# Kernel tuning notes

Measured on AMD Instinct MI355X. Metric: run time of the kernel, lower is better.

The kernel has to match this reference:

```python
import jax, jax.numpy as jnp
import numpy as np

EMBED_DIM = 256
IDX = 3
SLOT_NORM = True
NEG = -9e15


def setup_inputs() -> dict:
    key = jax.random.key(0)
    ks = jax.random.split(key, 7)
    B, S, D, N = 16, 8192, EMBED_DIM, 64
    return {
        "input_embedding": jax.random.normal(ks[0], (B, S, D), dtype=jnp.float32),
        "mask": jax.random.randint(ks[1], (B, N, S), 0, 2, dtype=jnp.int32),
        "Wv": jax.random.normal(ks[2], (D, D), dtype=jnp.float32) * 0.02,
        "bv": jax.random.normal(ks[3], (D,), dtype=jnp.float32) * 0.02,
        "Wk": jax.random.normal(ks[4], (D, D), dtype=jnp.float32) * 0.02,
        "bk": jax.random.normal(ks[5], (D,), dtype=jnp.float32) * 0.02,
        "queries": jax.random.normal(ks[6], (N, D), dtype=jnp.float32) * 0.02,
    }


def reference(input_embedding, mask, Wv, bv, Wk, bk, queries):
    # values/keys: [B, S, D] (torch Linear: x @ W.T + b)
    values = jnp.einsum("bsd,ed->bse", input_embedding, Wv) + bv
    keys = jnp.einsum("bsd,ed->bse", input_embedding, Wk) + bk
    # attn_logits: [B, N, S]
    logits = jnp.einsum("nd,bsd->bns", queries, keys) / jnp.sqrt(
        jnp.asarray(EMBED_DIM, dtype=keys.dtype)
    )
    logits = jnp.where(mask == 0, jnp.asarray(NEG, dtype=logits.dtype), logits)
    if SLOT_NORM:
        attn = jax.nn.softmax(logits, axis=-2)  # normalize over slots
        attn = attn / jnp.sum(attn, axis=-1, keepdims=True)
    else:
        attn = jax.nn.softmax(logits, axis=-1)
    attention = attn[:, IDX, :][:, None, :]  # [B, 1, S]
    out = jnp.matmul(attention, values)  # [B, 1, D]
    return out, attention
```

## Files before the change

kernel.cpp:

```cpp
#include <hip/hip_runtime.h>


#define B_ 16
#define S_ 8192
#define D_ 256
#define N_ 64
#define NEG_ (-9e15f)
#define LSTR 264

typedef __attribute__((ext_vector_type(8))) short s8_t;
typedef __attribute__((ext_vector_type(4))) float f4_t;
typedef unsigned int u32;
typedef unsigned short u16;

__device__ __forceinline__ u16 f2bf(float f) {
  u32 u = __builtin_bit_cast(u32, f);
  u += 0x7fffu + ((u >> 16) & 1u);
  return (u16)(u >> 16);
}
__device__ __forceinline__ float bflo(u32 p) { return __builtin_bit_cast(float, p << 16); }
__device__ __forceinline__ float bfhi(u32 p) { return __builtin_bit_cast(float, p & 0xffff0000u); }

__global__ void prep_qk(const float* __restrict__ queries, const float* __restrict__ Wk,
                        const float* __restrict__ bk, u16* __restrict__ qp,
                        float* __restrict__ qb) {
  const int n = blockIdx.x, d = threadIdx.x;
  const float* q = &queries[n * D_];
  float acc = 0.f;
  for (int e = 0; e < D_; ++e) acc = fmaf(q[e], Wk[e * D_ + d], acc);
  qp[n * D_ + d] = f2bf(acc);
  if (d == 0) {
    float s = 0.f;
    for (int e = 0; e < D_; ++e) s = fmaf(q[e], bk[e], s);
    qb[n] = s;
  }
}

__global__ __launch_bounds__(256, 2) void attn_main(
    const float* __restrict__ x, const int* __restrict__ mask,
    const u16* __restrict__ qp, const float* __restrict__ qb,
    float* __restrict__ wsum, float* __restrict__ denom, float* __restrict__ att) {
  __shared__ u16 q_lds[N_ * LSTR];
  __shared__ u16 in_lds[64 * LSTR];
  __shared__ u32 pm[4 * 64];

  const int t = threadIdx.x;
  const int lane = t & 63;
  const int w = t >> 6;
  const int c15 = lane & 15;
  const int g = lane >> 4;
  const int b = blockIdx.y;
  const int sbase = blockIdx.x * 256;

  {
    const int n = t >> 2, q = t & 3;
#pragma unroll
    for (int j = 0; j < 8; ++j)
      *(uint4*)&q_lds[n * LSTR + q * 64 + j * 8] = *(const uint4*)&qp[n * D_ + q * 64 + j * 8];
  }
  float qbv[4];
#pragma unroll
  for (int t4 = 0; t4 < 4; ++t4) qbv[t4] = qb[t4 * 16 + c15];

  f4_t wacc = {0.f, 0.f, 0.f, 0.f};
  float dacc = 0.f;

  for (int tt = 0; tt < 4; ++tt) {
    const int s0 = sbase + tt * 64;
    __syncthreads();
    {
      const int col = (t & 63) * 4;
#pragma unroll
      for (int it = 0; it < 16; ++it) {
        const int row = it * 4 + w;
        const float4 v = *(const float4*)&x[(((long)b * S_) + s0 + row) * D_ + col];
        uint2 h;
        h.x = (u32)f2bf(v.x) | ((u32)f2bf(v.y) << 16);
        h.y = (u32)f2bf(v.z) | ((u32)f2bf(v.w) << 16);
        *(uint2*)&in_lds[row * LSTR + col] = h;
      }
      const int s = t & 63, p = t >> 6;
      const int* mrow = mask + ((long)b * N_ + p * 16) * S_ + s0 + s;
      u32 bits = 0;
#pragma unroll
      for (int i = 0; i < 16; ++i) bits |= (u32)(mrow[i * S_] != 0) << i;
      pm[p * 64 + s] = bits;
    }
    __syncthreads();

    f4_t acc[4] = {{0.f,0.f,0.f,0.f},{0.f,0.f,0.f,0.f},{0.f,0.f,0.f,0.f},{0.f,0.f,0.f,0.f}};
    const u16* arow = &in_lds[(16 * w + c15) * LSTR + g * 8];
    const u16* br0 = &q_lds[(0 + c15) * LSTR + g * 8];
    const u16* br1 = &q_lds[(16 + c15) * LSTR + g * 8];
    const u16* br2 = &q_lds[(32 + c15) * LSTR + g * 8];
    const u16* br3 = &q_lds[(48 + c15) * LSTR + g * 8];
#pragma unroll
    for (int c = 0; c < 8; ++c) {
      const s8_t a = *(const s8_t*)&arow[c * 32];
      acc[0] = __builtin_amdgcn_mfma_f32_16x16x32_bf16(a, *(const s8_t*)&br0[c * 32], acc[0], 0, 0, 0);
      acc[1] = __builtin_amdgcn_mfma_f32_16x16x32_bf16(a, *(const s8_t*)&br1[c * 32], acc[1], 0, 0, 0);
      acc[2] = __builtin_amdgcn_mfma_f32_16x16x32_bf16(a, *(const s8_t*)&br2[c * 32], acc[2], 0, 0, 0);
      acc[3] = __builtin_amdgcn_mfma_f32_16x16x32_bf16(a, *(const s8_t*)&br3[c * 32], acc[3], 0, 0, 0);
    }

    float unorm[4];
#pragma unroll
    for (int r = 0; r < 4; ++r) {
      const int sl = 16 * w + g * 4 + r;
      float lf[4];
#pragma unroll
      for (int t4 = 0; t4 < 4; ++t4)
        lf[t4] = ((pm[t4 * 64 + sl] >> c15) & 1) ? (acc[t4][r] + qbv[t4]) * 0.0625f : NEG_;
      float m = fmaxf(fmaxf(lf[0], lf[1]), fmaxf(lf[2], lf[3]));
      m = fmaxf(m, __shfl_xor(m, 1));
      m = fmaxf(m, __shfl_xor(m, 2));
      m = fmaxf(m, __shfl_xor(m, 4));
      m = fmaxf(m, __shfl_xor(m, 8));
      const float e0 = __expf(lf[0] - m);
      float sm = e0 + __expf(lf[1] - m) + __expf(lf[2] - m) + __expf(lf[3] - m);
      sm += __shfl_xor(sm, 1);
      sm += __shfl_xor(sm, 2);
      sm += __shfl_xor(sm, 4);
      sm += __shfl_xor(sm, 8);
      const float e3 = __shfl(e0, (lane & 48) | 3);
      unorm[r] = e3 / sm;
    }
    if (c15 == 3) {
      f4_t u = {unorm[0], unorm[1], unorm[2], unorm[3]};
      *(f4_t*)&att[(long)b * S_ + s0 + 16 * w + g * 4] = u;
    }
#pragma unroll
    for (int r = 0; r < 4; ++r) {
#pragma unroll
      for (int gg = 0; gg < 4; ++gg) {
        const float a_s = __shfl(unorm[r], gg * 16);
        const uint2 h = *(const uint2*)&in_lds[(16 * w + gg * 4 + r) * LSTR + lane * 4];
        wacc[0] = fmaf(a_s, bflo(h.x), wacc[0]);
        wacc[1] = fmaf(a_s, bfhi(h.x), wacc[1]);
        wacc[2] = fmaf(a_s, bflo(h.y), wacc[2]);
        wacc[3] = fmaf(a_s, bfhi(h.y), wacc[3]);
        dacc += a_s;
      }
    }
  }
#pragma unroll
  for (int j = 0; j < 4; ++j) atomicAdd(&wsum[b * D_ + lane * 4 + j], wacc[j]);
  if (lane == 0) atomicAdd(&denom[b], dacc);
}

__global__ void finalize_k(const float* __restrict__ wsum, const float* __restrict__ denom,
                           const float* __restrict__ Wv, const float* __restrict__ bv,
                           float* __restrict__ out, float* __restrict__ att) {
  __shared__ float wl[D_];
  const int b = blockIdx.x, t = threadIdx.x;
  wl[t] = wsum[b * D_ + t];
  __syncthreads();
  const float dn = denom[b];
  float o = 0.f;
  const float* wr = &Wv[t * D_];
  for (int e = 0; e < D_; ++e) o = fmaf(wl[e], wr[e], o);
  out[b * D_ + t] = o / dn + bv[t];
  const float inv = 1.0f / dn;
  for (int s = t; s < S_; s += 256) att[(long)b * S_ + s] *= inv;
}

extern "C" void kernel_launch(void* const* d_in, const int* in_sizes, int n_in,
                              void* d_out, int out_size, void* d_ws, size_t ws_size,
                              hipStream_t stream) {
  const float* x = (const float*)d_in[0];
  const int* mask = (const int*)d_in[1];
  const float* Wv = (const float*)d_in[2];
  const float* bv = (const float*)d_in[3];
  const float* Wk = (const float*)d_in[4];
  const float* bk = (const float*)d_in[5];
  const float* queries = (const float*)d_in[6];

  char* ws = (char*)d_ws;
  u16* qp = (u16*)ws;
  float* qb = (float*)(ws + 32768);
  float* wsum = (float*)(ws + 33024);
  float* denom = (float*)(ws + 49408);
  float* out = (float*)d_out;
  float* att = out + B_ * D_;

  hipMemsetAsync(wsum, 0, 16384 + 64, stream);
  prep_qk<<<N_, D_, 0, stream>>>(queries, Wk, bk, qp, qb);
  attn_main<<<dim3(32, B_), 256, 0, stream>>>(x, mask, qp, qb, wsum, denom, att);
  finalize_k<<<B_, D_, 0, stream>>>(wsum, denom, Wv, bv, out, att);
}
```

Baseline: 270.3 us.

## Double grid, drop query LDS staging, replace atomics with per-block partials

The main kernel now handles 128 positions per block instead of 256 and launches 64x16 blocks. The query matrix is pre-swizzled into MFMA fragment order so each lane reads its operands straight from global memory, which removes the query LDS buffer and raises occupancy to 4 blocks per CU. Global atomics and the memset are replaced by per-block partial sums that are reduced in LDS and written out, and finalize gains a second grid dimension so it can rescale attention in parallel. The prep kernel is restructured to use LDS and a tree reduction. In exchange, query fragments are re-read from global or cache by every block, and finalize must reduce 64 partials per batch.

```diff
diff --git a/kernel.cpp b/kernel.cpp
--- a/kernel.cpp
+++ b/kernel.cpp
@@ -22,27 +22,37 @@
 __device__ __forceinline__ float bfhi(u32 p) { return __builtin_bit_cast(float, p & 0xffff0000u); }
 
 __global__ void prep_qk(const float* __restrict__ queries, const float* __restrict__ Wk,
-                        const float* __restrict__ bk, u16* __restrict__ qp,
+                        const float* __restrict__ bk, u16* __restrict__ qf,
                         float* __restrict__ qb) {
+  __shared__ float ql[D_];
+  __shared__ float rb[D_];
   const int n = blockIdx.x, d = threadIdx.x;
-  const float* q = &queries[n * D_];
-  float acc = 0.f;
-  for (int e = 0; e < D_; ++e) acc = fmaf(q[e], Wk[e * D_ + d], acc);
-  qp[n * D_ + d] = f2bf(acc);
-  if (d == 0) {
-    float s = 0.f;
-    for (int e = 0; e < D_; ++e) s = fmaf(q[e], bk[e], s);
-    qb[n] = s;
+  const float qv = queries[n * D_ + d];
+  ql[d] = qv;
+  rb[d] = qv * bk[d];
+  __syncthreads();
+  float a0 = 0.f, a1 = 0.f, a2 = 0.f, a3 = 0.f;
+#pragma unroll 4
+  for (int e = 0; e < D_; e += 4) {
+    a0 = fmaf(ql[e + 0], Wk[(e + 0) * D_ + d], a0);
+    a1 = fmaf(ql[e + 1], Wk[(e + 1) * D_ + d], a1);
+    a2 = fmaf(ql[e + 2], Wk[(e + 2) * D_ + d], a2);
+    a3 = fmaf(ql[e + 3], Wk[(e + 3) * D_ + d], a3);
   }
-}
-
-__global__ __launch_bounds__(256, 2) void attn_main(
+  const float acc = (a0 + a1) + (a2 + a3);
+  const int t4 = n >> 4, c15 = n & 15, c = d >> 5, g = (d >> 3) & 3, j = d & 7;
+  qf[((t4 * 8 + c) * 64 + g * 16 + c15) * 8 + j] = f2bf(acc);
+  for (int s = 128; s > 0; s >>= 1) { __syncthreads(); if (d < s) rb[d] += rb[d + s]; }
+  if (d == 0) qb[n] = rb[0];
+}
+
+__global__ __launch_bounds__(256, 4) void attn_main(
     const float* __restrict__ x, const int* __restrict__ mask,
-    const u16* __restrict__ qp, const float* __restrict__ qb,
-    float* __restrict__ wsum, float* __restrict__ denom, float* __restrict__ att) {
-  __shared__ u16 q_lds[N_ * LSTR];
-  __shared__ u16 in_lds[64 * LSTR];
+    const u16* __restrict__ qf, const float* __restrict__ qb,
+    float* __restrict__ pw, float* __restrict__ dpart, float* __restrict__ att) {
+  __shared__ __align__(16) u16 in_lds[64 * LSTR];
   __shared__ u32 pm[4 * 64];
+  float* ldsW = (float*)in_lds;
 
   const int t = threadIdx.x;
   const int lane = t & 63;
@@ -50,22 +60,16 @@
   const int c15 = lane & 15;
   const int g = lane >> 4;
   const int b = blockIdx.y;
-  const int sbase = blockIdx.x * 256;
-
-  {
-    const int n = t >> 2, q = t & 3;
-#pragma unroll
-    for (int j = 0; j < 8; ++j)
-      *(uint4*)&q_lds[n * LSTR + q * 64 + j * 8] = *(const uint4*)&qp[n * D_ + q * 64 + j * 8];
-  }
-  float qbv[4];
-#pragma unroll
-  for (int t4 = 0; t4 < 4; ++t4) qbv[t4] = qb[t4 * 16 + c15];
+  const int sb = blockIdx.x;
+  const int sbase = sb * 128;
+
+  const float qbv0 = qb[c15], qbv1 = qb[16 + c15], qbv2 = qb[32 + c15], qbv3 = qb[48 + c15];
+  const s8_t* qfs = (const s8_t*)qf;
 
   f4_t wacc = {0.f, 0.f, 0.f, 0.f};
   float dacc = 0.f;
 
-  for (int tt = 0; tt < 4; ++tt) {
+  for (int tt = 0; tt < 2; ++tt) {
     const int s0 = sbase + tt * 64;
     __syncthreads();
     {
@@ -80,7 +84,7 @@
         *(uint2*)&in_lds[row * LSTR + col] = h;
       }
       const int s = t & 63, p = t >> 6;
-      const int* mrow = mask + ((long)b * N_ + p * 16) * S_ + s0 + s;
+      const int* mrow = mask + ((long)b * N_ + p * 16) * S_ + sbase + tt * 64 + s;
       u32 bits = 0;
 #pragma unroll
       for (int i = 0; i < 16; ++i) bits |= (u32)(mrow[i * S_] != 0) << i;
@@ -88,36 +92,39 @@
     }
     __syncthreads();
 
-    f4_t acc[4] = {{0.f,0.f,0.f,0.f},{0.f,0.f,0.f,0.f},{0.f,0.f,0.f,0.f},{0.f,0.f,0.f,0.f}};
     const u16* arow = &in_lds[(16 * w + c15) * LSTR + g * 8];
-    const u16* br0 = &q_lds[(0 + c15) * LSTR + g * 8];
-    const u16* br1 = &q_lds[(16 + c15) * LSTR + g * 8];
-    const u16* br2 = &q_lds[(32 + c15) * LSTR + g * 8];
-    const u16* br3 = &q_lds[(48 + c15) * LSTR + g * 8];
+    f4_t acc0 = {0.f,0.f,0.f,0.f}, acc1 = {0.f,0.f,0.f,0.f};
+    f4_t acc2 = {0.f,0.f,0.f,0.f}, acc3 = {0.f,0.f,0.f,0.f};
 #pragma unroll
     for (int c = 0; c < 8; ++c) {
-      const s8_t a = *(const s8_t*)&arow[c * 32];
-      acc[0] = __builtin_amdgcn_mfma_f32_16x16x32_bf16(a, *(const s8_t*)&br0[c * 32], acc[0], 0, 0, 0);
-      acc[1] = __builtin_amdgcn_mfma_f32_16x16x32_bf16(a, *(const s8_t*)&br1[c * 32], acc[1], 0, 0, 0);
-      acc[2] = __builtin_amdgcn_mfma_f32_16x16x32_bf16(a, *(const s8_t*)&br2[c * 32], acc[2], 0, 0, 0);
-      acc[3] = __builtin_amdgcn_mfma_f32_16x16x32_bf16(a, *(const s8_t*)&br3[c * 32], acc[3], 0, 0, 0);
+      const s8_t a  = *(const s8_t*)&arow[c * 32];
+      const s8_t b0 = qfs[(0 * 8 + c) * 64 + lane];
+      const s8_t b1 = qfs[(1 * 8 + c) * 64 + lane];
+      const s8_t b2 = qfs[(2 * 8 + c) * 64 + lane];
+      const s8_t b3 = qfs[(3 * 8 + c) * 64 + lane];
+      acc0 = __builtin_amdgcn_mfma_f32_16x16x32_bf16(a, b0, acc0, 0, 0, 0);
+      acc1 = __builtin_amdgcn_mfma_f32_16x16x32_bf16(a, b1, acc1, 0, 0, 0);
+      acc2 = __builtin_amdgcn_mfma_f32_16x16x32_bf16(a, b2, acc2, 0, 0, 0);
+      acc3 = __builtin_amdgcn_mfma_f32_16x16x32_bf16(a, b3, acc3, 0, 0, 0);
     }
 
     float unorm[4];
 #pragma unroll
     for (int r = 0; r < 4; ++r) {
       const int sl = 16 * w + g * 4 + r;
-      float lf[4];
-#pragma unroll
-      for (int t4 = 0; t4 < 4; ++t4)
-        lf[t4] = ((pm[t4 * 64 + sl] >> c15) & 1) ? (acc[t4][r] + qbv[t4]) * 0.0625f : NEG_;
-      float m = fmaxf(fmaxf(lf[0], lf[1]), fmaxf(lf[2], lf[3]));
+      const u32 m0 = pm[0 * 64 + sl], m1 = pm[1 * 64 + sl];
+      const u32 m2 = pm[2 * 64 + sl], m3 = pm[3 * 64 + sl];
+      const float lf0 = ((m0 >> c15) & 1) ? (acc0[r] + qbv0) * 0.0625f : NEG_;
+      const float lf1 = ((m1 >> c15) & 1) ? (acc1[r] + qbv1) * 0.0625f : NEG_;
+      const float lf2 = ((m2 >> c15) & 1) ? (acc2[r] + qbv2) * 0.0625f : NEG_;
+      const float lf3 = ((m3 >> c15) & 1) ? (acc3[r] + qbv3) * 0.0625f : NEG_;
+      float m = fmaxf(fmaxf(lf0, lf1), fmaxf(lf2, lf3));
       m = fmaxf(m, __shfl_xor(m, 1));
       m = fmaxf(m, __shfl_xor(m, 2));
       m = fmaxf(m, __shfl_xor(m, 4));
       m = fmaxf(m, __shfl_xor(m, 8));
-      const float e0 = __expf(lf[0] - m);
-      float sm = e0 + __expf(lf[1] - m) + __expf(lf[2] - m) + __expf(lf[3] - m);
+      const float e0 = __expf(lf0 - m);
+      float sm = e0 + __expf(lf1 - m) + __expf(lf2 - m) + __expf(lf3 - m);
       sm += __shfl_xor(sm, 1);
       sm += __shfl_xor(sm, 2);
       sm += __shfl_xor(sm, 4);
@@ -129,6 +136,7 @@
       f4_t u = {unorm[0], unorm[1], unorm[2], unorm[3]};
       *(f4_t*)&att[(long)b * S_ + s0 + 16 * w + g * 4] = u;
     }
+
 #pragma unroll
     for (int r = 0; r < 4; ++r) {
 #pragma unroll
@@ -143,25 +151,65 @@
       }
     }
   }
-#pragma unroll
-  for (int j = 0; j < 4; ++j) atomicAdd(&wsum[b * D_ + lane * 4 + j], wacc[j]);
-  if (lane == 0) atomicAdd(&denom[b], dacc);
-}
-
-__global__ void finalize_k(const float* __restrict__ wsum, const float* __restrict__ denom,
+
+  __syncthreads();
+  if (t < 64) { f4_t z = {0.f,0.f,0.f,0.f}; *(f4_t*)&ldsW[t * 4] = z; }
+  if (t == 64) ldsW[D_] = 0.f;
+  __syncthreads();
+#pragma unroll
+  for (int j = 0; j < 4; ++j) atomicAdd(&ldsW[lane * 4 + j], wacc[j]);
+  if (lane == 0) atomicAdd(&ldsW[D_], dacc);
+  __syncthreads();
+  const int blk = b * 64 + sb;
+  if (t < D_) pw[(long)blk * D_ + t] = ldsW[t];
+  if (t == 0) dpart[blk] = ldsW[D_];
+}
+
+__global__ void finalize_k(const float* __restrict__ pw, const float* __restrict__ dpart,
                            const float* __restrict__ Wv, const float* __restrict__ bv,
                            float* __restrict__ out, float* __restrict__ att) {
+  __shared__ float red[64];
   __shared__ float wl[D_];
-  const int b = blockIdx.x, t = threadIdx.x;
-  wl[t] = wsum[b * D_ + t];
-  __syncthreads();
-  const float dn = denom[b];
-  float o = 0.f;
-  const float* wr = &Wv[t * D_];
-  for (int e = 0; e < D_; ++e) o = fmaf(wl[e], wr[e], o);
-  out[b * D_ + t] = o / dn + bv[t];
-  const float inv = 1.0f / dn;
-  for (int s = t; s < S_; s += 256) att[(long)b * S_ + s] *= inv;
+  const int b = blockIdx.x, t = threadIdx.x, part = blockIdx.y;
+  if (t < 64) red[t] = dpart[b * 64 + t];
+  __syncthreads();
+  if (t < 32) red[t] += red[t + 32];
+  __syncthreads();
+  if (t < 16) red[t] += red[t + 16];
+  __syncthreads();
+  if (t < 8) red[t] += red[t + 8];
+  __syncthreads();
+  if (t < 4) red[t] += red[t + 4];
+  __syncthreads();
+  if (t < 2) red[t] += red[t + 2];
+  __syncthreads();
+  if (t == 0) red[0] += red[1];
+  __syncthreads();
+  const float dn = red[0];
+  if (part == 0) {
+    float s0 = 0.f, s1 = 0.f, s2 = 0.f, s3 = 0.f;
+    const float* p = pw + (long)b * 64 * D_ + t;
+#pragma unroll 4
+    for (int sb = 0; sb < 64; sb += 4) {
+      s0 += p[(sb + 0) * D_]; s1 += p[(sb + 1) * D_];
+      s2 += p[(sb + 2) * D_]; s3 += p[(sb + 3) * D_];
+    }
+    wl[t] = (s0 + s1) + (s2 + s3);
+    __syncthreads();
+    const float4* wr = (const float4*)&Wv[t * D_];
+    const float4* wv = (const float4*)wl;
+    float d0 = 0.f, d1 = 0.f, d2 = 0.f, d3 = 0.f;
+#pragma unroll 8
+    for (int e = 0; e < 64; ++e) {
+      const float4 a = wv[e], w4 = wr[e];
+      d0 = fmaf(a.x, w4.x, d0); d1 = fmaf(a.y, w4.y, d1);
+      d2 = fmaf(a.z, w4.z, d2); d3 = fmaf(a.w, w4.w, d3);
+    }
+    out[b * D_ + t] = ((d0 + d1) + (d2 + d3)) / dn + bv[t];
+  } else {
+    const float inv = 1.0f / dn;
+    att[(long)b * S_ + (part - 1) * 256 + t] *= inv;
+  }
 }
 
 extern "C" void kernel_launch(void* const* d_in, const int* in_sizes, int n_in,
@@ -176,15 +224,14 @@
   const float* queries = (const float*)d_in[6];
 
   char* ws = (char*)d_ws;
-  u16* qp = (u16*)ws;
+  u16* qf = (u16*)ws;
   float* qb = (float*)(ws + 32768);
-  float* wsum = (float*)(ws + 33024);
-  float* denom = (float*)(ws + 49408);
+  float* pw = (float*)(ws + 33792);
+  float* dpart = (float*)(ws + 33792 + 1048576);
   float* out = (float*)d_out;
   float* att = out + B_ * D_;
 
-  hipMemsetAsync(wsum, 0, 16384 + 64, stream);
-  prep_qk<<<N_, D_, 0, stream>>>(queries, Wk, bk, qp, qb);
-  attn_main<<<dim3(32, B_), 256, 0, stream>>>(x, mask, qp, qb, wsum, denom, att);
-  finalize_k<<<B_, D_, 0, stream>>>(wsum, denom, Wv, bv, out, att);
-}
+  prep_qk<<<N_, D_, 0, stream>>>(queries, Wk, bk, qf, qb);
+  attn_main<<<dim3(64, B_), 256, 0, stream>>>(x, mask, qf, qb, pw, dpart, att);
+  finalize_k<<<dim3(B_, 33), 256, 0, stream>>>(pw, dpart, Wv, bv, out, att);
+}
```

Measured after the change: 323.2 us. +19.6%, slower.
